# Kernel optimization log

Hardware: AMD Instinct MI355X
Metric: run time of the kernel (lower is better)

Reference implementation:

```python
import jax, jax.numpy as jnp
from jax import lax
import numpy as np

B, N1, N2 = 4, 2048, 8192
C1, C2, K, F = 128, 64, 15, 128
NSAMPLE = 16
RADIUS = 0.2
KP_EXTEND = 1.0
EXTENT = KP_EXTEND * RADIUS  # area of influence of each kernel point


def setup_inputs() -> dict:
    key = jax.random.key(0)
    k0, k1, k2, k3, k4 = jax.random.split(key, 5)
    xyz1 = jax.random.uniform(k0, (B, N1, 3), dtype=jnp.float32)
    xyz2 = jax.random.uniform(k1, (B, N2, 3), dtype=jnp.float32)
    features1 = jax.random.normal(k2, (B, N1, C1), dtype=jnp.float32)
    features2 = jax.random.normal(k3, (B, N2, C2), dtype=jnp.float32)
    # Kernel points: fixed disposition inside a sphere of RADIUS, first point at
    # center (fixed='center'). Stands in for the offline potential-optimization.
    rng = np.random.RandomState(42)
    dirs = rng.randn(K, 3)
    dirs /= (np.linalg.norm(dirs, axis=1, keepdims=True) + 1e-9)
    rad = rng.rand(K, 1) ** (1.0 / 3.0)
    kp = dirs * rad
    kp[0, :] = 0.0  # fixed center point
    kernel_points = jnp.asarray(kp * RADIUS, dtype=jnp.float32)  # (K, 3)
    # Convolution kernel weights: one C1->F matrix per kernel point.
    W = jax.random.normal(k4, (K, C1, F), dtype=jnp.float32) * 0.05
    return {"xyz1": xyz1, "features1": features1, "xyz2": xyz2,
            "features2": features2, "kernel_points": kernel_points, "W": W}


def reference(xyz1, features1, xyz2, features2, kernel_points, W):
    # kNN search: for each query point in set 2, NSAMPLE nearest points in set 1.
    d2 = jnp.sum((xyz2[:, :, None, :] - xyz1[:, None, :, :]) ** 2, axis=-1)  # (B,N2,N1)
    _, idx = lax.top_k(-d2, NSAMPLE)  # (B, N2, S)
    # Irregular gather of neighbor coordinates and features.
    gather = jax.vmap(lambda arr, i: arr[i])  # per-batch fancy gather
    neigh_xyz = gather(xyz1, idx)        # (B, N2, S, 3)
    neigh_feat = gather(features1, idx)  # (B, N2, S, C1)
    # Neighbor positions relative to the query (center) point.
    rel = neigh_xyz - xyz2[:, :, None, :]  # (B, N2, S, 3)
    # Distances from each neighbor to each kernel point.
    diff = rel[:, :, :, None, :] - kernel_points[None, None, None, :, :]  # (B,N2,S,K,3)
    sq = jnp.sum(diff * diff, axis=-1)                                    # (B,N2,S,K)
    dist = jnp.sqrt(jnp.maximum(sq, 1e-12))
    # Linear kernel-point influence, aggregation_mode='sum'.
    weights = jax.nn.relu(1.0 - dist / EXTENT)  # (B, N2, S, K)
    # Weighted aggregation of neighbor features per kernel point.
    wf = jnp.einsum('bnsk,bnsc->bnkc', weights, neigh_feat)  # (B, N2, K, C1)
    # Kernel point convolution: per-kernel-point linear map, summed over K.
    out = jnp.einsum('bnkc,kcf->bnf', wf, W)  # (B, N2, F)
    out = jax.nn.relu(out)
    # Feature propagation: concat with skip features of set 2 (use_xyz=False).
    return jnp.concatenate([out, features2], axis=-1)  # (B, N2, F + C2)
```

## Files before the change

### kernel.cpp

```cpp
#include <hip/hip_runtime.h>

#define B 4
#define N1 2048
#define N2 8192
#define C1 128
#define C2 64
#define K 15
#define F 128
#define S 16

__global__ __launch_bounds__(512) void knn_kernel(
    const float* __restrict__ xyz1, const float* __restrict__ xyz2,
    unsigned short* __restrict__ nn_idx) {
#pragma clang fp contract(off)
  __shared__ float sx[N1], sy[N1], sz[N1];
  __shared__ float s_cd[16][522];
  __shared__ unsigned short s_ci[16][522];
  const int b = blockIdx.y;
  const int q0 = blockIdx.x * 16;
  const int tid = threadIdx.x;

  const float* p1 = xyz1 + (size_t)b * N1 * 3;
  for (int i = tid; i < N1; i += 512) {
    sx[i] = p1[i * 3 + 0];
    sy[i] = p1[i * 3 + 1];
    sz[i] = p1[i * 3 + 2];
  }
  __syncthreads();

  const int wv = tid >> 6;
  const int lane = tid & 63;
  const int q = lane & 15;
  const int sub = lane >> 4;
  const float* p2 = xyz2 + ((size_t)b * N2 + q0 + q) * 3;
  const float qx = p2[0], qy = p2[1], qz = p2[2];

  float bd[S];
  int bi[S];
#pragma unroll
  for (int j = 0; j < S; ++j) { bd[j] = 3.4e38f; bi[j] = 0x7fffffff; }

  const int i0 = wv * 256 + sub;
  for (int ii = 0; ii < 64; ++ii) {
    const int i = i0 + (ii << 2);
    float dx = qx - sx[i];
    float dy = qy - sy[i];
    float dz = qz - sz[i];
    float d = dx * dx;
    d = d + dy * dy;
    d = d + dz * dz;
    if (d < bd[S - 1]) {
      bd[S - 1] = d;
      bi[S - 1] = i;
#pragma unroll
      for (int j = S - 1; j > 0; --j) {
        if (bd[j] < bd[j - 1]) {
          float td = bd[j]; bd[j] = bd[j - 1]; bd[j - 1] = td;
          int ti = bi[j]; bi[j] = bi[j - 1]; bi[j - 1] = ti;
        }
      }
    }
  }
  {
    const int ls = (wv * 4 + sub) * 16;
#pragma unroll
    for (int j = 0; j < S; ++j) {
      s_cd[q][ls + j] = bd[j];
      s_ci[q][ls + j] = (unsigned short)bi[j];
    }
  }
  __syncthreads();

  for (int L = 32; L >= 4; L >>= 1) {
    const int half = L >> 1;
    const int nact = 16 * half;
    const int valid = tid < nact;
    float od[16];
    int oi[16];
    int q2 = 0, m = 0;
    if (valid) {
      q2 = tid / half;
      m = tid - q2 * half;
      int pa = (2 * m) * 16, ea = pa + 16;
      int pb = ea, eb = pb + 16;
#pragma unroll
      for (int j = 0; j < 16; ++j) {
        const int a_ok = pa < ea, b_ok = pb < eb;
        const int ra = a_ok ? pa : ea - 1;
        const int rb = b_ok ? pb : eb - 1;
        float da = s_cd[q2][ra];
        int ia = (int)s_ci[q2][ra];
        float db = s_cd[q2][rb];
        int ib = (int)s_ci[q2][rb];
        const int ta = a_ok && (!b_ok || da < db || (da == db && ia < ib));
        od[j] = ta ? da : db;
        oi[j] = ta ? ia : ib;
        pa += ta;
        pb += !ta;
      }
    }
    __syncthreads();
    if (valid) {
#pragma unroll
      for (int j = 0; j < 16; ++j) {
        s_cd[q2][m * 16 + j] = od[j];
        s_ci[q2][m * 16 + j] = (unsigned short)oi[j];
      }
    }
    __syncthreads();
  }

  if (tid < 16) {
    const int q2 = tid;
    int pa = 0, ea = 16, pb = 16, eb = 32;
    unsigned short* op = nn_idx + ((size_t)b * N2 + q0 + q2) * S;
#pragma unroll
    for (int j = 0; j < 16; ++j) {
      const int a_ok = pa < ea, b_ok = pb < eb;
      const int ra = a_ok ? pa : ea - 1;
      const int rb = b_ok ? pb : eb - 1;
      float da = s_cd[q2][ra];
      int ia = (int)s_ci[q2][ra];
      float db = s_cd[q2][rb];
      int ib = (int)s_ci[q2][rb];
      const int ta = a_ok && (!b_ok || da < db || (da == db && ia < ib));
      op[j] = (unsigned short)(ta ? ia : ib);
      pa += ta;
      pb += !ta;
    }
  }
}

__global__ __launch_bounds__(256) void conv_kernel(
    const float* __restrict__ xyz1, const float* __restrict__ feat1,
    const float* __restrict__ xyz2, const float* __restrict__ feat2,
    const float* __restrict__ kp, const float* __restrict__ W,
    const unsigned short* __restrict__ nn_idx, float* __restrict__ out) {
  __shared__ __align__(16) float s_buf[8448];
  int (*s_idx)[S] = (int(*)[S])(s_buf);
  float (*s_rel)[S][3] = (float(*)[S][3])(s_buf + 256);
  float (*s_w)[260] = (float(*)[260])(s_buf + 1024);
  float (*s_red)[16][132] = (float(*)[16][132])(s_buf);
  __shared__ float s_wf[C1][20];
  __shared__ float s_kp[K * 3];

  const int b = blockIdx.y;
  const int q0 = blockIdx.x * 16;
  const int tid = threadIdx.x;

  if (tid < K * 3) s_kp[tid] = kp[tid];
  s_idx[tid >> 4][tid & 15] = (int)nn_idx[((size_t)b * N2 + q0) * S + tid];
  __syncthreads();

  {
    int q = tid >> 4, s = tid & 15;
    int i = s_idx[q][s];
    const float* pn = xyz1 + ((size_t)b * N1 + i) * 3;
    const float* pq = xyz2 + ((size_t)b * N2 + q0 + q) * 3;
    s_rel[q][s][0] = pn[0] - pq[0];
    s_rel[q][s][1] = pn[1] - pq[1];
    s_rel[q][s][2] = pn[2] - pq[2];
  }
  __syncthreads();

  for (int t = tid; t < 16 * S * K; t += 256) {
    int q = t / (S * K);
    int r = t - q * (S * K);
    int s = r / K;
    int k = r - s * K;
    float rx = s_rel[q][s][0] - s_kp[k * 3 + 0];
    float ry = s_rel[q][s][1] - s_kp[k * 3 + 1];
    float rz = s_rel[q][s][2] - s_kp[k * 3 + 2];
    float d = sqrtf(fmaxf(rx * rx + ry * ry + rz * rz, 1e-12f));
    s_w[q][s * 16 + k] = fmaxf(0.0f, 1.0f - d / 0.2f);
  }
  __syncthreads();

  const int q = tid & 15;
  const int cg = tid >> 4;

  float wfr[K][8];
#pragma unroll
  for (int k = 0; k < K; ++k)
#pragma unroll
    for (int j = 0; j < 8; ++j) wfr[k][j] = 0.0f;

  for (int s = 0; s < S; ++s) {
    int i = s_idx[q][s];
    const float4* fp = (const float4*)(feat1 + ((size_t)b * N1 + i) * C1) + cg * 2;
    float4 n0 = fp[0];
    float4 n1 = fp[1];
    const float4* wr = (const float4*)(&s_w[q][s * 16]);
    float4 w0 = wr[0], w1 = wr[1], w2 = wr[2], w3 = wr[3];
    float wk[16] = {w0.x, w0.y, w0.z, w0.w, w1.x, w1.y, w1.z, w1.w,
                    w2.x, w2.y, w2.z, w2.w, w3.x, w3.y, w3.z, w3.w};
#pragma unroll
    for (int k = 0; k < K; ++k) {
      float w = wk[k];
      wfr[k][0] += w * n0.x;
      wfr[k][1] += w * n0.y;
      wfr[k][2] += w * n0.z;
      wfr[k][3] += w * n0.w;
      wfr[k][4] += w * n1.x;
      wfr[k][5] += w * n1.y;
      wfr[k][6] += w * n1.z;
      wfr[k][7] += w * n1.w;
    }
  }

  const int qg = tid >> 7;
  const int cs = (tid >> 5) & 3;
  const int fg = tid & 31;
  float4 acc[8];
#pragma unroll
  for (int qi = 0; qi < 8; ++qi) acc[qi] = make_float4(0.f, 0.f, 0.f, 0.f);

  for (int k = 0; k < K; ++k) {
    __syncthreads();
#pragma unroll
    for (int j = 0; j < 8; ++j) s_wf[cg * 8 + j][q] = wfr[k][j];
    __syncthreads();

    const float4* Wk4 = (const float4*)(W + (size_t)k * C1 * F) + fg;
#pragma unroll 4
    for (int c2 = 0; c2 < 32; ++c2) {
      int c = cs * 32 + c2;
      float4 wa = *(const float4*)(&s_wf[c][qg * 8 + 0]);
      float4 wb = *(const float4*)(&s_wf[c][qg * 8 + 4]);
      float4 w4 = Wk4[c * 32];
      acc[0].x += wa.x * w4.x; acc[0].y += wa.x * w4.y;
      acc[0].z += wa.x * w4.z; acc[0].w += wa.x * w4.w;
      acc[1].x += wa.y * w4.x; acc[1].y += wa.y * w4.y;
      acc[1].z += wa.y * w4.z; acc[1].w += wa.y * w4.w;
      acc[2].x += wa.z * w4.x; acc[2].y += wa.z * w4.y;
      acc[2].z += wa.z * w4.z; acc[2].w += wa.z * w4.w;
      acc[3].x += wa.w * w4.x; acc[3].y += wa.w * w4.y;
      acc[3].z += wa.w * w4.z; acc[3].w += wa.w * w4.w;
      acc[4].x += wb.x * w4.x; acc[4].y += wb.x * w4.y;
      acc[4].z += wb.x * w4.z; acc[4].w += wb.x * w4.w;
      acc[5].x += wb.y * w4.x; acc[5].y += wb.y * w4.y;
      acc[5].z += wb.y * w4.z; acc[5].w += wb.y * w4.w;
      acc[6].x += wb.z * w4.x; acc[6].y += wb.z * w4.y;
      acc[6].z += wb.z * w4.z; acc[6].w += wb.z * w4.w;
      acc[7].x += wb.w * w4.x; acc[7].y += wb.w * w4.y;
      acc[7].z += wb.w * w4.z; acc[7].w += wb.w * w4.w;
    }
  }

#pragma unroll
  for (int qi = 0; qi < 8; ++qi)
    *(float4*)(&s_red[cs][qg * 8 + qi][fg * 4]) = acc[qi];
  __syncthreads();

  for (int t = tid; t < 512; t += 256) {
    int qq = t >> 5;
    int fj = t & 31;
    float4 a0 = *(const float4*)&s_red[0][qq][fj * 4];
    float4 a1 = *(const float4*)&s_red[1][qq][fj * 4];
    float4 a2 = *(const float4*)&s_red[2][qq][fj * 4];
    float4 a3 = *(const float4*)&s_red[3][qq][fj * 4];
    float4 v;
    v.x = fmaxf(a0.x + a1.x + a2.x + a3.x, 0.0f);
    v.y = fmaxf(a0.y + a1.y + a2.y + a3.y, 0.0f);
    v.z = fmaxf(a0.z + a1.z + a2.z + a3.z, 0.0f);
    v.w = fmaxf(a0.w + a1.w + a2.w + a3.w, 0.0f);
    ((float4*)(out + ((size_t)b * N2 + q0 + qq) * (F + C2)))[fj] = v;
  }

  {
    int qq = tid >> 4;
    int j = tid & 15;
    float4 v = ((const float4*)(feat2 + ((size_t)b * N2 + q0 + qq) * C2))[j];
    ((float4*)(out + ((size_t)b * N2 + q0 + qq) * (F + C2) + F))[j] = v;
  }
}

extern "C" void kernel_launch(void* const* d_in, const int* in_sizes, int n_in,
                              void* d_out, int out_size, void* d_ws, size_t ws_size,
                              hipStream_t stream) {
  const float* xyz1 = (const float*)d_in[0];
  const float* feat1 = (const float*)d_in[1];
  const float* xyz2 = (const float*)d_in[2];
  const float* feat2 = (const float*)d_in[3];
  const float* kp = (const float*)d_in[4];
  const float* Wm = (const float*)d_in[5];
  float* out = (float*)d_out;

  unsigned short* nn_idx = (unsigned short*)d_ws;

  knn_kernel<<<dim3(N2 / 16, B), 512, 0, stream>>>(xyz1, xyz2, nn_idx);
  conv_kernel<<<dim3(N2 / 16, B), 256, 0, stream>>>(xyz1, feat1, xyz2, feat2,
                                                    kp, Wm, nn_idx, out);
}
```

Baseline: 543.1 us.

## Process 32 queries per conv block with K-chunked aggregation and shuffle reduction

The conv kernel now handles 32 query points per 512-thread block, so each W row loaded from global memory serves twice as many queries. Neighbor aggregation is split into three chunks of 5 kernel points, which cuts live accumulator registers but re-gathers the neighbor features three times. The cross-channel-slice reduction now uses a wave shuffle plus a smaller LDS exchange instead of a full LDS reduction buffer. The launch bound of 512 threads with a minimum of 4 blocks may force register spills. The larger LDS footprint may also limit how many blocks fit on a CU.

Measured after the change: 1.599 ms. +194.5%, slower.

```diff
diff --git a/kernel.cpp b/kernel.cpp
--- a/kernel.cpp
+++ b/kernel.cpp
@@ -131,21 +131,20 @@
   }
 }
 
-__global__ __launch_bounds__(256) void conv_kernel(
+__global__ __launch_bounds__(512, 4) void conv_kernel(
     const float* __restrict__ xyz1, const float* __restrict__ feat1,
     const float* __restrict__ xyz2, const float* __restrict__ feat2,
     const float* __restrict__ kp, const float* __restrict__ W,
     const unsigned short* __restrict__ nn_idx, float* __restrict__ out) {
-  __shared__ __align__(16) float s_buf[8448];
-  int (*s_idx)[S] = (int(*)[S])(s_buf);
-  float (*s_rel)[S][3] = (float(*)[S][3])(s_buf + 256);
-  float (*s_w)[260] = (float(*)[260])(s_buf + 1024);
-  float (*s_red)[16][132] = (float(*)[16][132])(s_buf);
-  __shared__ float s_wf[C1][20];
+  __shared__ int s_idx[32][S];
+  __shared__ float s_rel[32][S][3];
+  __shared__ float s_w[32][260];
+  __shared__ float s_wf[C1][36];
+  __shared__ float s_part[4][8][132];
   __shared__ float s_kp[K * 3];
 
   const int b = blockIdx.y;
-  const int q0 = blockIdx.x * 16;
+  const int q0 = blockIdx.x * 32;
   const int tid = threadIdx.x;
 
   if (tid < K * 3) s_kp[tid] = kp[tid];
@@ -163,7 +162,7 @@
   }
   __syncthreads();
 
-  for (int t = tid; t < 16 * S * K; t += 256) {
+  for (int t = tid; t < 32 * S * K; t += 512) {
     int q = t / (S * K);
     int r = t - q * (S * K);
     int s = r / K;
@@ -176,95 +175,111 @@
   }
   __syncthreads();
 
-  const int q = tid & 15;
-  const int cg = tid >> 4;
-
-  float wfr[K][8];
-#pragma unroll
-  for (int k = 0; k < K; ++k)
-#pragma unroll
-    for (int j = 0; j < 8; ++j) wfr[k][j] = 0.0f;
-
-  for (int s = 0; s < S; ++s) {
-    int i = s_idx[q][s];
-    const float4* fp = (const float4*)(feat1 + ((size_t)b * N1 + i) * C1) + cg * 2;
-    float4 n0 = fp[0];
-    float4 n1 = fp[1];
-    const float4* wr = (const float4*)(&s_w[q][s * 16]);
-    float4 w0 = wr[0], w1 = wr[1], w2 = wr[2], w3 = wr[3];
-    float wk[16] = {w0.x, w0.y, w0.z, w0.w, w1.x, w1.y, w1.z, w1.w,
-                    w2.x, w2.y, w2.z, w2.w, w3.x, w3.y, w3.z, w3.w};
-#pragma unroll
-    for (int k = 0; k < K; ++k) {
-      float w = wk[k];
-      wfr[k][0] += w * n0.x;
-      wfr[k][1] += w * n0.y;
-      wfr[k][2] += w * n0.z;
-      wfr[k][3] += w * n0.w;
-      wfr[k][4] += w * n1.x;
-      wfr[k][5] += w * n1.y;
-      wfr[k][6] += w * n1.z;
-      wfr[k][7] += w * n1.w;
-    }
-  }
-
+  const int q = tid & 31;
+  const int cg = tid >> 5;
   const int qg = tid >> 7;
   const int cs = (tid >> 5) & 3;
   const int fg = tid & 31;
+
   float4 acc[8];
 #pragma unroll
   for (int qi = 0; qi < 8; ++qi) acc[qi] = make_float4(0.f, 0.f, 0.f, 0.f);
 
-  for (int k = 0; k < K; ++k) {
-    __syncthreads();
-#pragma unroll
-    for (int j = 0; j < 8; ++j) s_wf[cg * 8 + j][q] = wfr[k][j];
-    __syncthreads();
-
-    const float4* Wk4 = (const float4*)(W + (size_t)k * C1 * F) + fg;
+#pragma unroll
+  for (int kc = 0; kc < 3; ++kc) {
+    float wfr[5][8];
+#pragma unroll
+    for (int kk = 0; kk < 5; ++kk)
+#pragma unroll
+      for (int j = 0; j < 8; ++j) wfr[kk][j] = 0.0f;
+
+    for (int s = 0; s < S; ++s) {
+      int i = s_idx[q][s];
+      const float4* fp =
+          (const float4*)(feat1 + ((size_t)b * N1 + i) * C1) + cg * 2;
+      float4 n0 = fp[0];
+      float4 n1 = fp[1];
+      const float4* wr = (const float4*)(&s_w[q][s * 16]);
+      float4 w0 = wr[0], w1 = wr[1], w2 = wr[2], w3 = wr[3];
+      float wk[16] = {w0.x, w0.y, w0.z, w0.w, w1.x, w1.y, w1.z, w1.w,
+                      w2.x, w2.y, w2.z, w2.w, w3.x, w3.y, w3.z, w3.w};
+#pragma unroll
+      for (int kk = 0; kk < 5; ++kk) {
+        float w = wk[kc * 5 + kk];
+        wfr[kk][0] += w * n0.x;
+        wfr[kk][1] += w * n0.y;
+        wfr[kk][2] += w * n0.z;
+        wfr[kk][3] += w * n0.w;
+        wfr[kk][4] += w * n1.x;
+        wfr[kk][5] += w * n1.y;
+        wfr[kk][6] += w * n1.z;
+        wfr[kk][7] += w * n1.w;
+      }
+    }
+
+#pragma unroll
+    for (int kk = 0; kk < 5; ++kk) {
+      const int k = kc * 5 + kk;
+      __syncthreads();
+#pragma unroll
+      for (int j = 0; j < 8; ++j) s_wf[cg * 8 + j][q] = wfr[kk][j];
+      __syncthreads();
+
+      const float4* Wk4 = (const float4*)(W + (size_t)k * C1 * F) + fg;
 #pragma unroll 4
-    for (int c2 = 0; c2 < 32; ++c2) {
-      int c = cs * 32 + c2;
-      float4 wa = *(const float4*)(&s_wf[c][qg * 8 + 0]);
-      float4 wb = *(const float4*)(&s_wf[c][qg * 8 + 4]);
-      float4 w4 = Wk4[c * 32];
-      acc[0].x += wa.x * w4.x; acc[0].y += wa.x * w4.y;
-      acc[0].z += wa.x * w4.z; acc[0].w += wa.x * w4.w;
-      acc[1].x += wa.y * w4.x; acc[1].y += wa.y * w4.y;
-      acc[1].z += wa.y * w4.z; acc[1].w += wa.y * w4.w;
-      acc[2].x += wa.z * w4.x; acc[2].y += wa.z * w4.y;
-      acc[2].z += wa.z * w4.z; acc[2].w += wa.z * w4.w;
-      acc[3].x += wa.w * w4.x; acc[3].y += wa.w * w4.y;
-      acc[3].z += wa.w * w4.z; acc[3].w += wa.w * w4.w;
-      acc[4].x += wb.x * w4.x; acc[4].y += wb.x * w4.y;
-      acc[4].z += wb.x * w4.z; acc[4].w += wb.x * w4.w;
-      acc[5].x += wb.y * w4.x; acc[5].y += wb.y * w4.y;
-      acc[5].z += wb.y * w4.z; acc[5].w += wb.y * w4.w;
-      acc[6].x += wb.z * w4.x; acc[6].y += wb.z * w4.y;
-      acc[6].z += wb.z * w4.z; acc[6].w += wb.z * w4.w;
-      acc[7].x += wb.w * w4.x; acc[7].y += wb.w * w4.y;
-      acc[7].z += wb.w * w4.z; acc[7].w += wb.w * w4.w;
-    }
-  }
-
-#pragma unroll
-  for (int qi = 0; qi < 8; ++qi)
-    *(float4*)(&s_red[cs][qg * 8 + qi][fg * 4]) = acc[qi];
-  __syncthreads();
-
-  for (int t = tid; t < 512; t += 256) {
-    int qq = t >> 5;
-    int fj = t & 31;
-    float4 a0 = *(const float4*)&s_red[0][qq][fj * 4];
-    float4 a1 = *(const float4*)&s_red[1][qq][fj * 4];
-    float4 a2 = *(const float4*)&s_red[2][qq][fj * 4];
-    float4 a3 = *(const float4*)&s_red[3][qq][fj * 4];
-    float4 v;
-    v.x = fmaxf(a0.x + a1.x + a2.x + a3.x, 0.0f);
-    v.y = fmaxf(a0.y + a1.y + a2.y + a3.y, 0.0f);
-    v.z = fmaxf(a0.z + a1.z + a2.z + a3.z, 0.0f);
-    v.w = fmaxf(a0.w + a1.w + a2.w + a3.w, 0.0f);
-    ((float4*)(out + ((size_t)b * N2 + q0 + qq) * (F + C2)))[fj] = v;
+      for (int c2 = 0; c2 < 32; ++c2) {
+        int c = cs * 32 + c2;
+        float4 wa = *(const float4*)(&s_wf[c][qg * 8 + 0]);
+        float4 wb = *(const float4*)(&s_wf[c][qg * 8 + 4]);
+        float4 w4 = Wk4[c * 32];
+        acc[0].x += wa.x * w4.x; acc[0].y += wa.x * w4.y;
+        acc[0].z += wa.x * w4.z; acc[0].w += wa.x * w4.w;
+        acc[1].x += wa.y * w4.x; acc[1].y += wa.y * w4.y;
+        acc[1].z += wa.y * w4.z; acc[1].w += wa.y * w4.w;
+        acc[2].x += wa.z * w4.x; acc[2].y += wa.z * w4.y;
+        acc[2].z += wa.z * w4.z; acc[2].w += wa.z * w4.w;
+        acc[3].x += wa.w * w4.x; acc[3].y += wa.w * w4.y;
+        acc[3].z += wa.w * w4.z; acc[3].w += wa.w * w4.w;
+        acc[4].x += wb.x * w4.x; acc[4].y += wb.x * w4.y;
+        acc[4].z += wb.x * w4.z; acc[4].w += wb.x * w4.w;
+        acc[5].x += wb.y * w4.x; acc[5].y += wb.y * w4.y;
+        acc[5].z += wb.y * w4.z; acc[5].w += wb.y * w4.w;
+        acc[6].x += wb.z * w4.x; acc[6].y += wb.z * w4.y;
+        acc[6].z += wb.z * w4.z; acc[6].w += wb.z * w4.w;
+        acc[7].x += wb.w * w4.x; acc[7].y += wb.w * w4.y;
+        acc[7].z += wb.w * w4.z; acc[7].w += wb.w * w4.w;
+      }
+    }
+  }
+
+#pragma unroll
+  for (int qi = 0; qi < 8; ++qi) {
+    acc[qi].x += __shfl_xor(acc[qi].x, 32, 64);
+    acc[qi].y += __shfl_xor(acc[qi].y, 32, 64);
+    acc[qi].z += __shfl_xor(acc[qi].z, 32, 64);
+    acc[qi].w += __shfl_xor(acc[qi].w, 32, 64);
+  }
+
+  const int wv = tid >> 6;
+  const int lane = tid & 63;
+  __syncthreads();
+  if ((wv & 1) && lane < 32) {
+#pragma unroll
+    for (int qi = 0; qi < 8; ++qi)
+      *(float4*)(&s_part[qg][qi][fg * 4]) = acc[qi];
+  }
+  __syncthreads();
+  if (!(wv & 1) && lane < 32) {
+#pragma unroll
+    for (int qi = 0; qi < 8; ++qi) {
+      float4 p = *(const float4*)(&s_part[qg][qi][fg * 4]);
+      float4 v;
+      v.x = fmaxf(acc[qi].x + p.x, 0.0f);
+      v.y = fmaxf(acc[qi].y + p.y, 0.0f);
+      v.z = fmaxf(acc[qi].z + p.z, 0.0f);
+      v.w = fmaxf(acc[qi].w + p.w, 0.0f);
+      ((float4*)(out + ((size_t)b * N2 + q0 + qg * 8 + qi) * (F + C2)))[fg] = v;
+    }
   }
 
   {
@@ -289,6 +304,6 @@
   unsigned short* nn_idx = (unsigned short*)d_ws;
 
   knn_kernel<<<dim3(N2 / 16, B), 512, 0, stream>>>(xyz1, xyz2, nn_idx);
-  conv_kernel<<<dim3(N2 / 16, B), 256, 0, stream>>>(xyz1, feat1, xyz2, feat2,
+  conv_kernel<<<dim3(N2 / 32, B), 512, 0, stream>>>(xyz1, feat1, xyz2, feat2,
                                                     kp, Wm, nn_idx, out);
 }
```
